# Kernel tuning notes

Measured on AMD Instinct MI355X. Metric: run time of the kernel, lower is better.

The kernel has to match this reference:

```python
import jax, jax.numpy as jnp
import numpy as np

TIME_STEP = 0.02  # matches init_kwargs
B, T, D = 128, 2048, 4


def setup_inputs() -> dict:
    key = jax.random.key(0)
    k1, k2, k3, k4 = jax.random.split(key, 4)
    return {
        "h_real": jax.random.normal(k1, (B, T, D, D), dtype=jnp.float32),
        "h_imag": jax.random.normal(k2, (B, T, D, D), dtype=jnp.float32),
        "s_real": jax.random.normal(k3, (B, D, D), dtype=jnp.float32),
        "s_imag": jax.random.normal(k4, (B, D, D), dtype=jnp.float32),
    }


def reference(h_real, h_imag, s_real, s_imag):
    # dt = -1j * time_step (complex64 scalar, as in the keras cell)
    dt = jnp.asarray(-1j * TIME_STEP, dtype=jnp.complex64)
    H = (h_real + 1j * h_imag).astype(jnp.complex64)        # [B,T,D,D]
    state0 = (s_real + 1j * s_imag).astype(jnp.complex64)    # [B,D,D]
    Hs = jnp.transpose(H, (1, 0, 2, 3))                       # [T,B,D,D] for scan

    def step(state, h_t):
        # unitary = expm(-i*dt*H_t), batched over B via expm's leading-dim batching
        unitary = jax.scipy.linalg.expm(h_t * dt)             # [B,D,D]
        new_state = jnp.matmul(unitary, state)                # [B,D,D]
        return new_state, new_state

    _, seq = jax.lax.scan(step, state0, Hs)                   # seq: [T,B,D,D] complex64
    # return real/imag stacked so downstream harness sees a real tensor
    return jnp.stack([seq.real, seq.imag])                    # [2,T,B,D,D] float32
```

## Files before the change

kernel.cpp:

```cpp
#include <hip/hip_runtime.h>

namespace {

constexpr int    TT     = 2048;
constexpr int    BB     = 128;
constexpr int    CHUNK  = 16;
constexpr int    NCHUNK = TT / CHUNK;
constexpr float  DT     = 0.02f;
constexpr size_t HALF   = (size_t)TT * BB * 16;

__device__ __forceinline__ void cmm(const float* __restrict__ ar, const float* __restrict__ ai,
                                    const float* __restrict__ br, const float* __restrict__ bi,
                                    float* __restrict__ cr, float* __restrict__ ci) {
#pragma unroll
    for (int i = 0; i < 4; ++i) {
#pragma unroll
        for (int j = 0; j < 4; ++j) {
            float sr = 0.f, si = 0.f;
#pragma unroll
            for (int k = 0; k < 4; ++k) {
                const float xr = ar[i * 4 + k], xi = ai[i * 4 + k];
                const float yr = br[k * 4 + j], yi = bi[k * 4 + j];
                sr = fmaf(xr, yr, sr);
                sr = fmaf(-xi, yi, sr);
                si = fmaf(xr, yi, si);
                si = fmaf(xi, yr, si);
            }
            cr[i * 4 + j] = sr;
            ci[i * 4 + j] = si;
        }
    }
}

}

__global__ __launch_bounds__(256) void kA_expm_scan(const float* __restrict__ hr,
                                                    const float* __restrict__ hi,
                                                    float* __restrict__ out,
                                                    float* __restrict__ totals) {
    const int gid  = blockIdx.x * 256 + threadIdx.x;
    const int sub  = gid & (CHUNK - 1);
    const int cid  = gid >> 4;
    const int b    = cid >> 7;
    const int c    = cid & (NCHUNK - 1);
    const int t    = c * CHUNK + sub;
    const int lane = threadIdx.x & 63;

    float a_r[16], a_i[16];
    {
        const size_t ho = ((size_t)b * TT + t) * 16;
        const float4* p4r = reinterpret_cast<const float4*>(hr + ho);
        const float4* p4i = reinterpret_cast<const float4*>(hi + ho);
#pragma unroll
        for (int v = 0; v < 4; ++v) {
            const float4 r  = p4r[v];
            const float4 im = p4i[v];
            a_r[v * 4 + 0] = DT * im.x;  a_i[v * 4 + 0] = -DT * r.x;
            a_r[v * 4 + 1] = DT * im.y;  a_i[v * 4 + 1] = -DT * r.y;
            a_r[v * 4 + 2] = DT * im.z;  a_i[v * 4 + 2] = -DT * r.z;
            a_r[v * 4 + 3] = DT * im.w;  a_i[v * 4 + 3] = -DT * r.w;
        }
    }

    float a2r[16], a2i[16], a3r[16], a3i[16];
    cmm(a_r, a_i, a_r, a_i, a2r, a2i);
    cmm(a2r, a2i, a_r, a_i, a3r, a3i);

    float tr[16], ti[16];
#pragma unroll
    for (int e = 0; e < 16; ++e) {
        const float d = (e % 5 == 0) ? 1.0f : 0.0f;
        tr[e] = fmaf(a_r[e], 1.f / 24.f, d * (1.f / 6.f));
        tr[e] = fmaf(a2r[e], 1.f / 120.f, tr[e]);
        tr[e] = fmaf(a3r[e], 1.f / 720.f, tr[e]);
        ti[e] = a_i[e] * (1.f / 24.f);
        ti[e] = fmaf(a2i[e], 1.f / 120.f, ti[e]);
        ti[e] = fmaf(a3i[e], 1.f / 720.f, ti[e]);
    }

    float er[16], ei[16];
    cmm(a3r, a3i, tr, ti, er, ei);
#pragma unroll
    for (int e = 0; e < 16; ++e) {
        const float d = (e % 5 == 0) ? 1.0f : 0.0f;
        er[e] = er[e] + d + a_r[e] + 0.5f * a2r[e];
        ei[e] = ei[e] + a_i[e] + 0.5f * a2i[e];
    }

#pragma unroll
    for (int d = 1; d < CHUNK; d <<= 1) {
        int src = lane - d;
        if (src < 0) src = 0;
        float qr[16], qi[16];
#pragma unroll
        for (int e = 0; e < 16; ++e) {
            qr[e] = __shfl(er[e], src, 64);
            qi[e] = __shfl(ei[e], src, 64);
        }
        float nr[16], ni[16];
        cmm(er, ei, qr, qi, nr, ni);
        const bool pred = (sub >= d);
#pragma unroll
        for (int e = 0; e < 16; ++e) {
            er[e] = pred ? nr[e] : er[e];
            ei[e] = pred ? ni[e] : ei[e];
        }
    }

    {
        const size_t o = ((size_t)t * BB + b) * 16;
        float4* orp = reinterpret_cast<float4*>(out + o);
        float4* oip = reinterpret_cast<float4*>(out + HALF + o);
#pragma unroll
        for (int v = 0; v < 4; ++v) {
            orp[v] = make_float4(er[v * 4 + 0], er[v * 4 + 1], er[v * 4 + 2], er[v * 4 + 3]);
            oip[v] = make_float4(ei[v * 4 + 0], ei[v * 4 + 1], ei[v * 4 + 2], ei[v * 4 + 3]);
        }
    }

    if (sub == CHUNK - 1) {
        float* tp = totals + (size_t)cid * 32;
#pragma unroll
        for (int e = 0; e < 16; ++e) {
            tp[e]      = er[e];
            tp[16 + e] = ei[e];
        }
    }
}

__global__ __launch_bounds__(256) void kC_carry(const float* __restrict__ totals,
                                                const float* __restrict__ sr,
                                                const float* __restrict__ si,
                                                float* __restrict__ carry) {
    __shared__ float sRe[32][256];
    __shared__ float sIm[32][256];

    const int tid  = threadIdx.x;
    const int bloc = tid >> 7;
    const int ct   = tid & (NCHUNK - 1);
    const int b    = blockIdx.x * 2 + bloc;

    float pr[16], pi[16];
    if (ct == 0) {
#pragma unroll
        for (int e = 0; e < 16; ++e) {
            pr[e] = sr[b * 16 + e];
            pi[e] = si[b * 16 + e];
        }
    } else {
        const float* tp = totals + ((size_t)b * NCHUNK + (ct - 1)) * 32;
#pragma unroll
        for (int e = 0; e < 16; ++e) {
            pr[e] = tp[e];
            pi[e] = tp[16 + e];
        }
    }

#pragma unroll
    for (int e = 0; e < 16; ++e) {
        sRe[e][tid]      = pr[e];
        sIm[e][tid]      = pi[e];
        sRe[e + 16][tid] = 0.f;
        sIm[e + 16][tid] = 0.f;
    }
    __syncthreads();

#pragma unroll
    for (int d = 1; d < NCHUNK; d <<= 1) {
        int srcI = tid - d;
        if (ct < d) srcI = bloc << 7;
        float qr[16], qi[16];
#pragma unroll
        for (int e = 0; e < 16; ++e) {
            qr[e] = sRe[e][srcI];
            qi[e] = sIm[e][srcI];
        }
        float nr[16], ni[16];
        cmm(pr, pi, qr, qi, nr, ni);
        const bool pred = (ct >= d);
#pragma unroll
        for (int e = 0; e < 16; ++e) {
            pr[e] = pred ? nr[e] : pr[e];
            pi[e] = pred ? ni[e] : pi[e];
        }
        __syncthreads();
#pragma unroll
        for (int e = 0; e < 16; ++e) {
            sRe[e][tid] = pr[e];
            sIm[e][tid] = pi[e];
        }
        __syncthreads();
    }

    float* cp = carry + ((size_t)b * NCHUNK + ct) * 32;
#pragma unroll
    for (int e = 0; e < 16; ++e) {
        cp[e]      = pr[e];
        cp[16 + e] = pi[e];
    }
}

__global__ __launch_bounds__(256) void kD_final(float* __restrict__ buf,
                                                const float* __restrict__ carry) {
    const int gid = blockIdx.x * 256 + threadIdx.x;
    const int b = gid & (BB - 1);
    const int t = gid >> 7;
    const int c = t >> 4;

    const size_t o = (size_t)gid * 16;
    float l_r[16], l_i[16];
    {
        const float4* p4r = reinterpret_cast<const float4*>(buf + o);
        const float4* p4i = reinterpret_cast<const float4*>(buf + HALF + o);
#pragma unroll
        for (int v = 0; v < 4; ++v) {
            const float4 r  = p4r[v];
            const float4 im = p4i[v];
            l_r[v * 4 + 0] = r.x;  l_i[v * 4 + 0] = im.x;
            l_r[v * 4 + 1] = r.y;  l_i[v * 4 + 1] = im.y;
            l_r[v * 4 + 2] = r.z;  l_i[v * 4 + 2] = im.z;
            l_r[v * 4 + 3] = r.w;  l_i[v * 4 + 3] = im.w;
        }
    }

    float c_r[16], c_i[16];
    {
        const float* cp = carry + ((size_t)b * NCHUNK + c) * 32;
#pragma unroll
        for (int e = 0; e < 16; ++e) {
            c_r[e] = cp[e];
            c_i[e] = cp[16 + e];
        }
    }

    float o_r[16], o_i[16];
    cmm(l_r, l_i, c_r, c_i, o_r, o_i);

    float4* orp = reinterpret_cast<float4*>(buf + o);
    float4* oip = reinterpret_cast<float4*>(buf + HALF + o);
#pragma unroll
    for (int v = 0; v < 4; ++v) {
        orp[v] = make_float4(o_r[v * 4 + 0], o_r[v * 4 + 1], o_r[v * 4 + 2], o_r[v * 4 + 3]);
        oip[v] = make_float4(o_i[v * 4 + 0], o_i[v * 4 + 1], o_i[v * 4 + 2], o_i[v * 4 + 3]);
    }
}

extern "C" void kernel_launch(void* const* d_in, const int* in_sizes, int n_in,
                              void* d_out, int out_size, void* d_ws, size_t ws_size,
                              hipStream_t stream) {
    const float* hr = (const float*)d_in[0];
    const float* hi = (const float*)d_in[1];
    const float* sr = (const float*)d_in[2];
    const float* si = (const float*)d_in[3];
    float* out    = (float*)d_out;
    float* totals = (float*)d_ws;
    float* carry  = (float*)d_ws + (size_t)BB * NCHUNK * 32;

    kA_expm_scan<<<(BB * TT) / 256, 256, 0, stream>>>(hr, hi, out, totals);
    kC_carry    <<<BB / 2, 256, 0, stream>>>(totals, sr, si, carry);
    kD_final    <<<(BB * TT) / 256, 256, 0, stream>>>(out, carry);
}
```

Baseline: 134.2 us.

## Store chunk scans in b-major workspace and transpose to output through LDS

The expm/scan kernel now writes its local prefix products contiguously in input order ([B,T]) to a workspace instead of scattering them into the [T,B] output layout. The carry kernel reads chunk totals directly from that workspace, so the separate totals buffer goes away. The final kernel tiles 16 t by 16 b, applies the carry, and transposes through padded shared memory so the [T,B] output writes are coalesced. This is meant to avoid strided global writes, at the cost of a 2*HALF workspace buffer and an extra LDS round trip with a barrier.

Result: no change. 132.9 us (-1.0%).

```diff
diff --git a/kernel.cpp b/kernel.cpp
--- a/kernel.cpp
+++ b/kernel.cpp
@@ -36,21 +36,16 @@
 
 __global__ __launch_bounds__(256) void kA_expm_scan(const float* __restrict__ hr,
                                                     const float* __restrict__ hi,
-                                                    float* __restrict__ out,
-                                                    float* __restrict__ totals) {
+                                                    float* __restrict__ L) {
     const int gid  = blockIdx.x * 256 + threadIdx.x;
-    const int sub  = gid & (CHUNK - 1);
-    const int cid  = gid >> 4;
-    const int b    = cid >> 7;
-    const int c    = cid & (NCHUNK - 1);
-    const int t    = c * CHUNK + sub;
+    const int t    = gid & (TT - 1);
+    const int sub  = t & (CHUNK - 1);
     const int lane = threadIdx.x & 63;
 
     float a_r[16], a_i[16];
     {
-        const size_t ho = ((size_t)b * TT + t) * 16;
-        const float4* p4r = reinterpret_cast<const float4*>(hr + ho);
-        const float4* p4i = reinterpret_cast<const float4*>(hi + ho);
+        const float4* p4r = reinterpret_cast<const float4*>(hr) + (size_t)gid * 4;
+        const float4* p4i = reinterpret_cast<const float4*>(hi) + (size_t)gid * 4;
 #pragma unroll
         for (int v = 0; v < 4; ++v) {
             const float4 r  = p4r[v];
@@ -66,25 +61,26 @@
     cmm(a_r, a_i, a_r, a_i, a2r, a2i);
     cmm(a2r, a2i, a_r, a_i, a3r, a3i);
 
-    float tr[16], ti[16];
-#pragma unroll
-    for (int e = 0; e < 16; ++e) {
-        const float d = (e % 5 == 0) ? 1.0f : 0.0f;
-        tr[e] = fmaf(a_r[e], 1.f / 24.f, d * (1.f / 6.f));
-        tr[e] = fmaf(a2r[e], 1.f / 120.f, tr[e]);
-        tr[e] = fmaf(a3r[e], 1.f / 720.f, tr[e]);
-        ti[e] = a_i[e] * (1.f / 24.f);
-        ti[e] = fmaf(a2i[e], 1.f / 120.f, ti[e]);
-        ti[e] = fmaf(a3i[e], 1.f / 720.f, ti[e]);
-    }
-
     float er[16], ei[16];
-    cmm(a3r, a3i, tr, ti, er, ei);
-#pragma unroll
-    for (int e = 0; e < 16; ++e) {
-        const float d = (e % 5 == 0) ? 1.0f : 0.0f;
-        er[e] = er[e] + d + a_r[e] + 0.5f * a2r[e];
-        ei[e] = ei[e] + a_i[e] + 0.5f * a2i[e];
+    {
+        float tr[16], ti[16];
+#pragma unroll
+        for (int e = 0; e < 16; ++e) {
+            const float d = (e % 5 == 0) ? 1.0f : 0.0f;
+            tr[e] = fmaf(a_r[e], 1.f / 24.f, d * (1.f / 6.f));
+            tr[e] = fmaf(a2r[e], 1.f / 120.f, tr[e]);
+            tr[e] = fmaf(a3r[e], 1.f / 720.f, tr[e]);
+            ti[e] = a_i[e] * (1.f / 24.f);
+            ti[e] = fmaf(a2i[e], 1.f / 120.f, ti[e]);
+            ti[e] = fmaf(a3i[e], 1.f / 720.f, ti[e]);
+        }
+        cmm(a3r, a3i, tr, ti, er, ei);
+#pragma unroll
+        for (int e = 0; e < 16; ++e) {
+            const float d = (e % 5 == 0) ? 1.0f : 0.0f;
+            er[e] = er[e] + d + a_r[e] + 0.5f * a2r[e];
+            ei[e] = ei[e] + a_i[e] + 0.5f * a2i[e];
+        }
     }
 
 #pragma unroll
@@ -108,32 +104,22 @@
     }
 
     {
-        const size_t o = ((size_t)t * BB + b) * 16;
-        float4* orp = reinterpret_cast<float4*>(out + o);
-        float4* oip = reinterpret_cast<float4*>(out + HALF + o);
+        float4* orp = reinterpret_cast<float4*>(L) + (size_t)gid * 4;
+        float4* oip = reinterpret_cast<float4*>(L + HALF) + (size_t)gid * 4;
 #pragma unroll
         for (int v = 0; v < 4; ++v) {
             orp[v] = make_float4(er[v * 4 + 0], er[v * 4 + 1], er[v * 4 + 2], er[v * 4 + 3]);
             oip[v] = make_float4(ei[v * 4 + 0], ei[v * 4 + 1], ei[v * 4 + 2], ei[v * 4 + 3]);
         }
     }
-
-    if (sub == CHUNK - 1) {
-        float* tp = totals + (size_t)cid * 32;
-#pragma unroll
-        for (int e = 0; e < 16; ++e) {
-            tp[e]      = er[e];
-            tp[16 + e] = ei[e];
-        }
-    }
-}
-
-__global__ __launch_bounds__(256) void kC_carry(const float* __restrict__ totals,
+}
+
+__global__ __launch_bounds__(256) void kC_carry(const float* __restrict__ L,
                                                 const float* __restrict__ sr,
                                                 const float* __restrict__ si,
                                                 float* __restrict__ carry) {
-    __shared__ float sRe[32][256];
-    __shared__ float sIm[32][256];
+    __shared__ float sRe[16][256];
+    __shared__ float sIm[16][256];
 
     const int tid  = threadIdx.x;
     const int bloc = tid >> 7;
@@ -148,20 +134,18 @@
             pi[e] = si[b * 16 + e];
         }
     } else {
-        const float* tp = totals + ((size_t)b * NCHUNK + (ct - 1)) * 32;
-#pragma unroll
-        for (int e = 0; e < 16; ++e) {
-            pr[e] = tp[e];
-            pi[e] = tp[16 + e];
+        const size_t o = ((size_t)b * TT + (size_t)ct * CHUNK - 1) * 16;
+#pragma unroll
+        for (int e = 0; e < 16; ++e) {
+            pr[e] = L[o + e];
+            pi[e] = L[HALF + o + e];
         }
     }
 
 #pragma unroll
     for (int e = 0; e < 16; ++e) {
-        sRe[e][tid]      = pr[e];
-        sIm[e][tid]      = pi[e];
-        sRe[e + 16][tid] = 0.f;
-        sIm[e + 16][tid] = 0.f;
+        sRe[e][tid] = pr[e];
+        sIm[e][tid] = pi[e];
     }
     __syncthreads();
 
@@ -200,18 +184,24 @@
     }
 }
 
-__global__ __launch_bounds__(256) void kD_final(float* __restrict__ buf,
-                                                const float* __restrict__ carry) {
-    const int gid = blockIdx.x * 256 + threadIdx.x;
-    const int b = gid & (BB - 1);
-    const int t = gid >> 7;
-    const int c = t >> 4;
-
-    const size_t o = (size_t)gid * 16;
-    float l_r[16], l_i[16];
-    {
-        const float4* p4r = reinterpret_cast<const float4*>(buf + o);
-        const float4* p4i = reinterpret_cast<const float4*>(buf + HALF + o);
+__global__ __launch_bounds__(256) void kD_final(const float* __restrict__ L,
+                                                const float* __restrict__ carry,
+                                                float* __restrict__ out) {
+    __shared__ float lds[32 * 16 * 17];
+
+    const int bid   = blockIdx.x;
+    const int tileT = bid & (NCHUNK - 1);
+    const int tileB = bid >> 7;
+    const int t0 = tileT * 16, b0 = tileB * 16;
+    const int tid = threadIdx.x;
+
+    {
+        const int bloc = tid >> 4, tloc = tid & 15;
+        const size_t li = ((size_t)(b0 + bloc) * TT + (t0 + tloc)) * 16;
+
+        float l_r[16], l_i[16];
+        const float4* p4r = reinterpret_cast<const float4*>(L + li);
+        const float4* p4i = reinterpret_cast<const float4*>(L + HALF + li);
 #pragma unroll
         for (int v = 0; v < 4; ++v) {
             const float4 r  = p4r[v];
@@ -221,27 +211,47 @@
             l_r[v * 4 + 2] = r.z;  l_i[v * 4 + 2] = im.z;
             l_r[v * 4 + 3] = r.w;  l_i[v * 4 + 3] = im.w;
         }
-    }
-
-    float c_r[16], c_i[16];
-    {
-        const float* cp = carry + ((size_t)b * NCHUNK + c) * 32;
+
+        float c_r[16], c_i[16];
+        const float* cp = carry + ((size_t)(b0 + bloc) * NCHUNK + tileT) * 32;
 #pragma unroll
         for (int e = 0; e < 16; ++e) {
             c_r[e] = cp[e];
             c_i[e] = cp[16 + e];
         }
-    }
-
-    float o_r[16], o_i[16];
-    cmm(l_r, l_i, c_r, c_i, o_r, o_i);
-
-    float4* orp = reinterpret_cast<float4*>(buf + o);
-    float4* oip = reinterpret_cast<float4*>(buf + HALF + o);
-#pragma unroll
-    for (int v = 0; v < 4; ++v) {
-        orp[v] = make_float4(o_r[v * 4 + 0], o_r[v * 4 + 1], o_r[v * 4 + 2], o_r[v * 4 + 3]);
-        oip[v] = make_float4(o_i[v * 4 + 0], o_i[v * 4 + 1], o_i[v * 4 + 2], o_i[v * 4 + 3]);
+
+        float o_r[16], o_i[16];
+        cmm(l_r, l_i, c_r, c_i, o_r, o_i);
+
+        const int slot = bloc * 17 + tloc;
+#pragma unroll
+        for (int e = 0; e < 16; ++e) {
+            lds[e * 272 + slot]        = o_r[e];
+            lds[(e + 16) * 272 + slot] = o_i[e];
+        }
+    }
+    __syncthreads();
+
+    {
+        const int u = tid >> 4;
+        const int v = tid & 15;
+        const int slot = v * 17 + u;
+
+        float r2[16], i2[16];
+#pragma unroll
+        for (int e = 0; e < 16; ++e) {
+            r2[e] = lds[e * 272 + slot];
+            i2[e] = lds[(e + 16) * 272 + slot];
+        }
+
+        const size_t oi = ((size_t)(t0 + u) * BB + (b0 + v)) * 16;
+        float4* orp = reinterpret_cast<float4*>(out + oi);
+        float4* oip = reinterpret_cast<float4*>(out + HALF + oi);
+#pragma unroll
+        for (int w = 0; w < 4; ++w) {
+            orp[w] = make_float4(r2[w * 4 + 0], r2[w * 4 + 1], r2[w * 4 + 2], r2[w * 4 + 3]);
+            oip[w] = make_float4(i2[w * 4 + 0], i2[w * 4 + 1], i2[w * 4 + 2], i2[w * 4 + 3]);
+        }
     }
 }
 
@@ -252,11 +262,11 @@
     const float* hi = (const float*)d_in[1];
     const float* sr = (const float*)d_in[2];
     const float* si = (const float*)d_in[3];
-    float* out    = (float*)d_out;
-    float* totals = (float*)d_ws;
-    float* carry  = (float*)d_ws + (size_t)BB * NCHUNK * 32;
-
-    kA_expm_scan<<<(BB * TT) / 256, 256, 0, stream>>>(hr, hi, out, totals);
-    kC_carry    <<<BB / 2, 256, 0, stream>>>(totals, sr, si, carry);
-    kD_final    <<<(BB * TT) / 256, 256, 0, stream>>>(out, carry);
-}
+    float* out   = (float*)d_out;
+    float* L     = (float*)d_ws;
+    float* carry = (float*)d_ws + 2 * HALF;
+
+    kA_expm_scan<<<(BB * TT) / 256, 256, 0, stream>>>(hr, hi, L);
+    kC_carry    <<<BB / 2, 256, 0, stream>>>(L, sr, si, carry);
+    kD_final    <<<(BB * TT) / 256, 256, 0, stream>>>(L, carry, out);
+}
```

## Fuse expm, chunk scan, carry scan and fixup into one per-batch kernel

Applied to the files above, without the earlier changes.

Replaces the three-kernel pipeline (expm plus chunk scan, carry scan, final fixup) with one kernel that runs one 1024-thread block per batch element and walks the sequence in two rounds. Chunk totals and carries stay in shared memory, and a running base is passed between rounds, so the global round trip of the output buffer and two extra launches go away. The Taylor series for expm is also cut from order 6 to order 4, which removes one 4x4 complex matmul per step but lowers accuracy. The launch now has only 128 blocks of 1024 threads with serialized rounds, so parallelism and occupancy may be limited.

New measurement: 148.2 us. +10.5%, slower.

```diff
diff --git a/kernel.cpp b/kernel.cpp
--- a/kernel.cpp
+++ b/kernel.cpp
@@ -5,9 +5,12 @@
 constexpr int    TT     = 2048;
 constexpr int    BB     = 128;
 constexpr int    CHUNK  = 16;
-constexpr int    NCHUNK = TT / CHUNK;
+constexpr int    RLEN   = 1024;
+constexpr int    NCH    = RLEN / CHUNK;
+constexpr int    ROUNDS = TT / RLEN;
 constexpr float  DT     = 0.02f;
 constexpr size_t HALF   = (size_t)TT * BB * 16;
+constexpr int    PITCH  = 33;
 
 __device__ __forceinline__ void cmm(const float* __restrict__ ar, const float* __restrict__ ai,
                                     const float* __restrict__ br, const float* __restrict__ bi,
@@ -34,214 +37,165 @@
 
 }
 
-__global__ __launch_bounds__(256) void kA_expm_scan(const float* __restrict__ hr,
-                                                    const float* __restrict__ hi,
-                                                    float* __restrict__ out,
-                                                    float* __restrict__ totals) {
-    const int gid  = blockIdx.x * 256 + threadIdx.x;
-    const int sub  = gid & (CHUNK - 1);
-    const int cid  = gid >> 4;
-    const int b    = cid >> 7;
-    const int c    = cid & (NCHUNK - 1);
-    const int t    = c * CHUNK + sub;
-    const int lane = threadIdx.x & 63;
-
-    float a_r[16], a_i[16];
-    {
-        const size_t ho = ((size_t)b * TT + t) * 16;
-        const float4* p4r = reinterpret_cast<const float4*>(hr + ho);
-        const float4* p4i = reinterpret_cast<const float4*>(hi + ho);
+__global__ __launch_bounds__(1024, 4) void kFused(const float* __restrict__ hr,
+                                                  const float* __restrict__ hi,
+                                                  const float* __restrict__ sr0,
+                                                  const float* __restrict__ si0,
+                                                  float* __restrict__ out) {
+    __shared__ float sTot[NCH * PITCH];
+    __shared__ float sCar[NCH * PITCH];
+    __shared__ float sBase[32];
+
+    const int tid   = threadIdx.x;
+    const int b     = blockIdx.x;
+    const int chunk = tid >> 4;
+    const int sub   = tid & 15;
+    const int lane  = tid & 63;
+
+    if (tid < 16) {
+        sBase[tid]      = sr0[b * 16 + tid];
+        sBase[16 + tid] = si0[b * 16 + tid];
+    }
+
+    for (int r = 0; r < ROUNDS; ++r) {
+        const int t = r * RLEN + tid;
+
+        float a_r[16], a_i[16];
+        {
+            const float4* p4r = reinterpret_cast<const float4*>(hr) + ((size_t)b * TT + t) * 4;
+            const float4* p4i = reinterpret_cast<const float4*>(hi) + ((size_t)b * TT + t) * 4;
+#pragma unroll
+            for (int v = 0; v < 4; ++v) {
+                const float4 rr = p4r[v];
+                const float4 im = p4i[v];
+                a_r[v * 4 + 0] = DT * im.x;  a_i[v * 4 + 0] = -DT * rr.x;
+                a_r[v * 4 + 1] = DT * im.y;  a_i[v * 4 + 1] = -DT * rr.y;
+                a_r[v * 4 + 2] = DT * im.z;  a_i[v * 4 + 2] = -DT * rr.z;
+                a_r[v * 4 + 3] = DT * im.w;  a_i[v * 4 + 3] = -DT * rr.w;
+            }
+        }
+
+        float er[16], ei[16];
+        {
+            float a2r[16], a2i[16];
+            cmm(a_r, a_i, a_r, a_i, a2r, a2i);
+            float tr[16], ti[16];
+#pragma unroll
+            for (int e = 0; e < 16; ++e) {
+                const float d = (e % 5 == 0) ? 1.0f : 0.0f;
+                tr[e] = fmaf(a_r[e], 1.f / 6.f, d * 0.5f);
+                tr[e] = fmaf(a2r[e], 1.f / 24.f, tr[e]);
+                ti[e] = a_i[e] * (1.f / 6.f);
+                ti[e] = fmaf(a2i[e], 1.f / 24.f, ti[e]);
+            }
+            cmm(a2r, a2i, tr, ti, er, ei);
+#pragma unroll
+            for (int e = 0; e < 16; ++e) {
+                const float d = (e % 5 == 0) ? 1.0f : 0.0f;
+                er[e] = er[e] + d + a_r[e];
+                ei[e] = ei[e] + a_i[e];
+            }
+        }
+
+#pragma unroll
+        for (int d = 1; d < CHUNK; d <<= 1) {
+            int src = lane - d;
+            if (src < 0) src = 0;
+            float qr[16], qi[16];
+#pragma unroll
+            for (int e = 0; e < 16; ++e) {
+                qr[e] = __shfl(er[e], src, 64);
+                qi[e] = __shfl(ei[e], src, 64);
+            }
+            float nr[16], ni[16];
+            cmm(er, ei, qr, qi, nr, ni);
+            const bool pred = (sub >= d);
+#pragma unroll
+            for (int e = 0; e < 16; ++e) {
+                er[e] = pred ? nr[e] : er[e];
+                ei[e] = pred ? ni[e] : ei[e];
+            }
+        }
+
+        if (sub == CHUNK - 1) {
+#pragma unroll
+            for (int e = 0; e < 16; ++e) {
+                sTot[chunk * PITCH + e]      = er[e];
+                sTot[chunk * PITCH + 16 + e] = ei[e];
+            }
+        }
+        __syncthreads();
+
+        if (tid < NCH) {
+            float mr[16], mi[16];
+            if (tid == 0) {
+#pragma unroll
+                for (int e = 0; e < 16; ++e) { mr[e] = sBase[e]; mi[e] = sBase[16 + e]; }
+            } else {
+#pragma unroll
+                for (int e = 0; e < 16; ++e) {
+                    mr[e] = sTot[(tid - 1) * PITCH + e];
+                    mi[e] = sTot[(tid - 1) * PITCH + 16 + e];
+                }
+            }
+#pragma unroll
+            for (int d = 1; d < NCH; d <<= 1) {
+                int src = lane - d;
+                if (src < 0) src = 0;
+                float qr[16], qi[16];
+#pragma unroll
+                for (int e = 0; e < 16; ++e) {
+                    qr[e] = __shfl(mr[e], src, 64);
+                    qi[e] = __shfl(mi[e], src, 64);
+                }
+                float nr[16], ni[16];
+                cmm(mr, mi, qr, qi, nr, ni);
+                const bool pred = (lane >= d);
+#pragma unroll
+                for (int e = 0; e < 16; ++e) {
+                    mr[e] = pred ? nr[e] : mr[e];
+                    mi[e] = pred ? ni[e] : mi[e];
+                }
+            }
+#pragma unroll
+            for (int e = 0; e < 16; ++e) {
+                sCar[tid * PITCH + e]      = mr[e];
+                sCar[tid * PITCH + 16 + e] = mi[e];
+            }
+            if (tid == NCH - 1) {
+                float t3r[16], t3i[16], nbr[16], nbi[16];
+#pragma unroll
+                for (int e = 0; e < 16; ++e) {
+                    t3r[e] = sTot[(NCH - 1) * PITCH + e];
+                    t3i[e] = sTot[(NCH - 1) * PITCH + 16 + e];
+                }
+                cmm(t3r, t3i, mr, mi, nbr, nbi);
+#pragma unroll
+                for (int e = 0; e < 16; ++e) {
+                    sBase[e]      = nbr[e];
+                    sBase[16 + e] = nbi[e];
+                }
+            }
+        }
+        __syncthreads();
+
+        float c_r[16], c_i[16];
+#pragma unroll
+        for (int e = 0; e < 16; ++e) {
+            c_r[e] = sCar[chunk * PITCH + e];
+            c_i[e] = sCar[chunk * PITCH + 16 + e];
+        }
+        float o_r[16], o_i[16];
+        cmm(er, ei, c_r, c_i, o_r, o_i);
+
+        const size_t oi = ((size_t)t * BB + b) * 16;
+        float4* orp = reinterpret_cast<float4*>(out + oi);
+        float4* oip = reinterpret_cast<float4*>(out + HALF + oi);
 #pragma unroll
         for (int v = 0; v < 4; ++v) {
-            const float4 r  = p4r[v];
-            const float4 im = p4i[v];
-            a_r[v * 4 + 0] = DT * im.x;  a_i[v * 4 + 0] = -DT * r.x;
-            a_r[v * 4 + 1] = DT * im.y;  a_i[v * 4 + 1] = -DT * r.y;
-            a_r[v * 4 + 2] = DT * im.z;  a_i[v * 4 + 2] = -DT * r.z;
-            a_r[v * 4 + 3] = DT * im.w;  a_i[v * 4 + 3] = -DT * r.w;
-        }
-    }
-
-    float a2r[16], a2i[16], a3r[16], a3i[16];
-    cmm(a_r, a_i, a_r, a_i, a2r, a2i);
-    cmm(a2r, a2i, a_r, a_i, a3r, a3i);
-
-    float tr[16], ti[16];
-#pragma unroll
-    for (int e = 0; e < 16; ++e) {
-        const float d = (e % 5 == 0) ? 1.0f : 0.0f;
-        tr[e] = fmaf(a_r[e], 1.f / 24.f, d * (1.f / 6.f));
-        tr[e] = fmaf(a2r[e], 1.f / 120.f, tr[e]);
-        tr[e] = fmaf(a3r[e], 1.f / 720.f, tr[e]);
-        ti[e] = a_i[e] * (1.f / 24.f);
-        ti[e] = fmaf(a2i[e], 1.f / 120.f, ti[e]);
-        ti[e] = fmaf(a3i[e], 1.f / 720.f, ti[e]);
-    }
-
-    float er[16], ei[16];
-    cmm(a3r, a3i, tr, ti, er, ei);
-#pragma unroll
-    for (int e = 0; e < 16; ++e) {
-        const float d = (e % 5 == 0) ? 1.0f : 0.0f;
-        er[e] = er[e] + d + a_r[e] + 0.5f * a2r[e];
-        ei[e] = ei[e] + a_i[e] + 0.5f * a2i[e];
-    }
-
-#pragma unroll
-    for (int d = 1; d < CHUNK; d <<= 1) {
-        int src = lane - d;
-        if (src < 0) src = 0;
-        float qr[16], qi[16];
-#pragma unroll
-        for (int e = 0; e < 16; ++e) {
-            qr[e] = __shfl(er[e], src, 64);
-            qi[e] = __shfl(ei[e], src, 64);
-        }
-        float nr[16], ni[16];
-        cmm(er, ei, qr, qi, nr, ni);
-        const bool pred = (sub >= d);
-#pragma unroll
-        for (int e = 0; e < 16; ++e) {
-            er[e] = pred ? nr[e] : er[e];
-            ei[e] = pred ? ni[e] : ei[e];
-        }
-    }
-
-    {
-        const size_t o = ((size_t)t * BB + b) * 16;
-        float4* orp = reinterpret_cast<float4*>(out + o);
-        float4* oip = reinterpret_cast<float4*>(out + HALF + o);
-#pragma unroll
-        for (int v = 0; v < 4; ++v) {
-            orp[v] = make_float4(er[v * 4 + 0], er[v * 4 + 1], er[v * 4 + 2], er[v * 4 + 3]);
-            oip[v] = make_float4(ei[v * 4 + 0], ei[v * 4 + 1], ei[v * 4 + 2], ei[v * 4 + 3]);
-        }
-    }
-
-    if (sub == CHUNK - 1) {
-        float* tp = totals + (size_t)cid * 32;
-#pragma unroll
-        for (int e = 0; e < 16; ++e) {
-            tp[e]      = er[e];
-            tp[16 + e] = ei[e];
-        }
-    }
-}
-
-__global__ __launch_bounds__(256) void kC_carry(const float* __restrict__ totals,
-                                                const float* __restrict__ sr,
-                                                const float* __restrict__ si,
-                                                float* __restrict__ carry) {
-    __shared__ float sRe[32][256];
-    __shared__ float sIm[32][256];
-
-    const int tid  = threadIdx.x;
-    const int bloc = tid >> 7;
-    const int ct   = tid & (NCHUNK - 1);
-    const int b    = blockIdx.x * 2 + bloc;
-
-    float pr[16], pi[16];
-    if (ct == 0) {
-#pragma unroll
-        for (int e = 0; e < 16; ++e) {
-            pr[e] = sr[b * 16 + e];
-            pi[e] = si[b * 16 + e];
-        }
-    } else {
-        const float* tp = totals + ((size_t)b * NCHUNK + (ct - 1)) * 32;
-#pragma unroll
-        for (int e = 0; e < 16; ++e) {
-            pr[e] = tp[e];
-            pi[e] = tp[16 + e];
-        }
-    }
-
-#pragma unroll
-    for (int e = 0; e < 16; ++e) {
-        sRe[e][tid]      = pr[e];
-        sIm[e][tid]      = pi[e];
-        sRe[e + 16][tid] = 0.f;
-        sIm[e + 16][tid] = 0.f;
-    }
-    __syncthreads();
-
-#pragma unroll
-    for (int d = 1; d < NCHUNK; d <<= 1) {
-        int srcI = tid - d;
-        if (ct < d) srcI = bloc << 7;
-        float qr[16], qi[16];
-#pragma unroll
-        for (int e = 0; e < 16; ++e) {
-            qr[e] = sRe[e][srcI];
-            qi[e] = sIm[e][srcI];
-        }
-        float nr[16], ni[16];
-        cmm(pr, pi, qr, qi, nr, ni);
-        const bool pred = (ct >= d);
-#pragma unroll
-        for (int e = 0; e < 16; ++e) {
-            pr[e] = pred ? nr[e] : pr[e];
-            pi[e] = pred ? ni[e] : pi[e];
-        }
-        __syncthreads();
-#pragma unroll
-        for (int e = 0; e < 16; ++e) {
-            sRe[e][tid] = pr[e];
-            sIm[e][tid] = pi[e];
-        }
-        __syncthreads();
-    }
-
-    float* cp = carry + ((size_t)b * NCHUNK + ct) * 32;
-#pragma unroll
-    for (int e = 0; e < 16; ++e) {
-        cp[e]      = pr[e];
-        cp[16 + e] = pi[e];
-    }
-}
-
-__global__ __launch_bounds__(256) void kD_final(float* __restrict__ buf,
-                                                const float* __restrict__ carry) {
-    const int gid = blockIdx.x * 256 + threadIdx.x;
-    const int b = gid & (BB - 1);
-    const int t = gid >> 7;
-    const int c = t >> 4;
-
-    const size_t o = (size_t)gid * 16;
-    float l_r[16], l_i[16];
-    {
-        const float4* p4r = reinterpret_cast<const float4*>(buf + o);
-        const float4* p4i = reinterpret_cast<const float4*>(buf + HALF + o);
-#pragma unroll
-        for (int v = 0; v < 4; ++v) {
-            const float4 r  = p4r[v];
-            const float4 im = p4i[v];
-            l_r[v * 4 + 0] = r.x;  l_i[v * 4 + 0] = im.x;
-            l_r[v * 4 + 1] = r.y;  l_i[v * 4 + 1] = im.y;
-            l_r[v * 4 + 2] = r.z;  l_i[v * 4 + 2] = im.z;
-            l_r[v * 4 + 3] = r.w;  l_i[v * 4 + 3] = im.w;
-        }
-    }
-
-    float c_r[16], c_i[16];
-    {
-        const float* cp = carry + ((size_t)b * NCHUNK + c) * 32;
-#pragma unroll
-        for (int e = 0; e < 16; ++e) {
-            c_r[e] = cp[e];
-            c_i[e] = cp[16 + e];
-        }
-    }
-
-    float o_r[16], o_i[16];
-    cmm(l_r, l_i, c_r, c_i, o_r, o_i);
-
-    float4* orp = reinterpret_cast<float4*>(buf + o);
-    float4* oip = reinterpret_cast<float4*>(buf + HALF + o);
-#pragma unroll
-    for (int v = 0; v < 4; ++v) {
-        orp[v] = make_float4(o_r[v * 4 + 0], o_r[v * 4 + 1], o_r[v * 4 + 2], o_r[v * 4 + 3]);
-        oip[v] = make_float4(o_i[v * 4 + 0], o_i[v * 4 + 1], o_i[v * 4 + 2], o_i[v * 4 + 3]);
+            orp[v] = make_float4(o_r[v * 4 + 0], o_r[v * 4 + 1], o_r[v * 4 + 2], o_r[v * 4 + 3]);
+            oip[v] = make_float4(o_i[v * 4 + 0], o_i[v * 4 + 1], o_i[v * 4 + 2], o_i[v * 4 + 3]);
+        }
     }
 }
 
@@ -252,11 +206,7 @@
     const float* hi = (const float*)d_in[1];
     const float* sr = (const float*)d_in[2];
     const float* si = (const float*)d_in[3];
-    float* out    = (float*)d_out;
-    float* totals = (float*)d_ws;
-    float* carry  = (float*)d_ws + (size_t)BB * NCHUNK * 32;
-
-    kA_expm_scan<<<(BB * TT) / 256, 256, 0, stream>>>(hr, hi, out, totals);
-    kC_carry    <<<BB / 2, 256, 0, stream>>>(totals, sr, si, carry);
-    kD_final    <<<(BB * TT) / 256, 256, 0, stream>>>(out, carry);
-}
+    float* out = (float*)d_out;
+
+    kFused<<<BB, RLEN, 0, stream>>>(hr, hi, sr, si, out);
+}
```
